# Optimization experiments

Measured on AMD Instinct MI355X. Metric: run time of the kernel, lower is better.

## Reference

```python
import jax, jax.numpy as jnp
import numpy as np

B, N, C = 32, 4096, 1152
TOPK_FRAC = 0.1


def setup_inputs() -> dict:
    key = jax.random.key(0)
    k1, k2 = jax.random.split(key)
    feature = jax.random.normal(k1, (B, N, C), dtype=jnp.float32)
    W = jax.random.normal(k2, (C,), dtype=jnp.float32) * 0.02  # conv1x1 weight [out=1, in=C, k=1] squeezed
    b = jnp.zeros((1,), dtype=jnp.float32)
    return {"feature": feature, "W": W, "b": b}


def reference(feature, W, b):
    # conv1x1 over [B, C, N] == per-patch dot product with W: [B, N]
    scores = jnp.einsum("bnc,c->bn", feature, W) + b[0]
    n = scores.shape[1]
    k = max(int(n * TOPK_FRAC), 1)  # static: 409
    topk_vals, _ = jax.lax.top_k(jnp.abs(scores), k)  # [B, k]
    per_sample = jnp.mean(topk_vals, axis=1)  # [B]
    # image_pyramid has a single level -> cat + mean over dim=1 is identity
    return [per_sample.reshape(-1, 1)]
```

## Files before the change

### kernel.cpp

```cpp
#include <hip/hip_runtime.h>

#define B_ 32
#define N_ 4096
#define C_ 1152
#define K_ 409

#define NBLK 2048
#define PATCH_PER_BLK ((B_ * N_) / NBLK)
#define ITERS (PATCH_PER_BLK / 4)

typedef float f32x4 __attribute__((ext_vector_type(4)));

__global__ __launch_bounds__(256) void score_abs_kernel(
    const float* __restrict__ feat, const float* __restrict__ W,
    const float* __restrict__ bias, float* __restrict__ absS) {
  __shared__ f32x4 Ws[C_ / 4];
  for (int i = threadIdx.x; i < C_ / 4; i += 256)
    Ws[i] = reinterpret_cast<const f32x4*>(W)[i];
  __syncthreads();

  const int wave = threadIdx.x >> 6;
  const int lane = threadIdx.x & 63;
  const float b0 = bias[0];

  const f32x4 w0 = Ws[lane];
  const f32x4 w1 = Ws[lane + 64];
  const f32x4 w2 = Ws[lane + 128];
  const f32x4 w3 = Ws[lane + 192];
  const f32x4 w4 = (lane < 32) ? Ws[lane + 256] : (f32x4)0.f;

  const int patch_base = blockIdx.x * PATCH_PER_BLK + wave;
#pragma unroll 4
  for (int it = 0; it < ITERS; ++it) {
    const int patch = patch_base + it * 4;
    const f32x4* f4 = reinterpret_cast<const f32x4*>(feat) + (size_t)patch * (C_ / 4);
    f32x4 vacc = __builtin_nontemporal_load(&f4[lane]) * w0;
    vacc += __builtin_nontemporal_load(&f4[lane + 64]) * w1;
    vacc += __builtin_nontemporal_load(&f4[lane + 128]) * w2;
    vacc += __builtin_nontemporal_load(&f4[lane + 192]) * w3;
    if (lane < 32) vacc += __builtin_nontemporal_load(&f4[lane + 256]) * w4;
    float acc = vacc[0] + vacc[1] + vacc[2] + vacc[3];
#pragma unroll
    for (int off = 32; off > 0; off >>= 1)
      acc += __shfl_down(acc, off, 64);
    if (lane == 0) absS[patch] = fabsf(acc + b0);
  }
}

__global__ __launch_bounds__(256) void topk_mean_kernel(
    const float* __restrict__ absS, float* __restrict__ out) {
  __shared__ float vals[N_];
  __shared__ unsigned hist[256];
  __shared__ unsigned cum[256];
  __shared__ unsigned s_sel[2];
  __shared__ unsigned s_cred[4];
  __shared__ float s_sredf[4];

  const int t = threadIdx.x;
  const int wv = t >> 6;
  const int ln = t & 63;
  const int b = blockIdx.x;
  const float4* row4 = reinterpret_cast<const float4*>(absS + (size_t)b * N_);
  for (int i = t; i < N_ / 4; i += 256)
    reinterpret_cast<float4*>(vals)[i] = row4[i];
  __syncthreads();

  unsigned prefix = 0;
  unsigned k = K_;
#pragma unroll
  for (int p = 0; p < 4; ++p) {
    const int shift = 24 - 8 * p;
    const unsigned hmask = (p == 0) ? 0u : (0xFFFFFFFFu << (shift + 8));
    hist[t] = 0;
    __syncthreads();
    for (int i = t; i < N_; i += 256) {
      const unsigned e = __float_as_uint(vals[i]);
      if ((e & hmask) == (prefix & hmask))
        atomicAdd(&hist[(e >> shift) & 255u], 1u);
    }
    __syncthreads();
    cum[t] = hist[t];
    __syncthreads();
#pragma unroll
    for (int off = 1; off < 256; off <<= 1) {
      const unsigned v = (t + off < 256) ? cum[t + off] : 0u;
      __syncthreads();
      cum[t] += v;
      __syncthreads();
    }
    const unsigned cnt_ge = cum[t];
    const unsigned cnt_gt = (t == 255) ? 0u : cum[t + 1];
    if (cnt_ge >= k && cnt_gt < k) {
      s_sel[0] = (unsigned)t;
      s_sel[1] = k - cnt_gt;
    }
    __syncthreads();
    prefix |= s_sel[0] << shift;
    k = s_sel[1];
    __syncthreads();
  }
  const float thr = __uint_as_float(prefix);

  float sum = 0.f;
  unsigned cgt = 0;
  for (int i = t; i < N_; i += 256) {
    const float v = vals[i];
    if (v > thr) { sum += v; cgt++; }
  }
#pragma unroll
  for (int off = 32; off > 0; off >>= 1) {
    sum += __shfl_down(sum, off, 64);
    cgt += __shfl_down(cgt, off, 64);
  }
  if (ln == 0) { s_cred[wv] = cgt; s_sredf[wv] = sum; }
  __syncthreads();
  if (t == 0) {
    const unsigned cg = s_cred[0] + s_cred[1] + s_cred[2] + s_cred[3];
    const float sg = s_sredf[0] + s_sredf[1] + s_sredf[2] + s_sredf[3];
    out[b] = (sg + (float)(K_ - (int)cg) * thr) / (float)K_;
  }
}

extern "C" void kernel_launch(void* const* d_in, const int* in_sizes, int n_in,
                              void* d_out, int out_size, void* d_ws, size_t ws_size,
                              hipStream_t stream) {
  const float* feat = (const float*)d_in[0];
  const float* W = (const float*)d_in[1];
  const float* bias = (const float*)d_in[2];
  float* out = (float*)d_out;
  float* absS = (float*)d_ws;

  score_abs_kernel<<<NBLK, 256, 0, stream>>>(feat, W, bias, absS);
  topk_mean_kernel<<<B_, 256, 0, stream>>>(absS, out);
}
```

Before: 108.2 us.

## Fuse scoring and top-k via last-block-per-row completion counter

New measurement: 322.3 us. 198% more time.

```diff
diff --git a/kernel.cpp b/kernel.cpp
--- a/kernel.cpp
+++ b/kernel.cpp
@@ -6,97 +6,116 @@
 #define K_ 409
 
 #define NBLK 2048
-#define PATCH_PER_BLK ((B_ * N_) / NBLK)
-#define ITERS (PATCH_PER_BLK / 4)
+#define PATCH_PER_BLK 64
+#define ITERS 16
+#define BLOCKS_PER_ROW 64
 
 typedef float f32x4 __attribute__((ext_vector_type(4)));
 
-__global__ __launch_bounds__(256) void score_abs_kernel(
+__global__ __launch_bounds__(256) void fused_kernel(
     const float* __restrict__ feat, const float* __restrict__ W,
-    const float* __restrict__ bias, float* __restrict__ absS) {
-  __shared__ f32x4 Ws[C_ / 4];
-  for (int i = threadIdx.x; i < C_ / 4; i += 256)
-    Ws[i] = reinterpret_cast<const f32x4*>(W)[i];
+    const float* __restrict__ bias, float* __restrict__ absS,
+    unsigned* __restrict__ cnt, float* __restrict__ out) {
+  __shared__ union {
+    f32x4 Ws[C_ / 4];
+    struct {
+      float vals[N_];
+      unsigned hist[256];
+      unsigned wsum[4];
+      unsigned sel[2];
+      float sredf[4];
+      unsigned cred[4];
+      int islast;
+    } tk;
+  } sh;
+
+  const int t = threadIdx.x;
+  const int wave = t >> 6;
+  const int lane = t & 63;
+
+  for (int i = t; i < C_ / 4; i += 256)
+    sh.Ws[i] = reinterpret_cast<const f32x4*>(W)[i];
   __syncthreads();
 
-  const int wave = threadIdx.x >> 6;
-  const int lane = threadIdx.x & 63;
   const float b0 = bias[0];
+  const f32x4 w0 = sh.Ws[lane];
+  const f32x4 w1 = sh.Ws[lane + 64];
+  const f32x4 w2 = sh.Ws[lane + 128];
+  const f32x4 w3 = sh.Ws[lane + 192];
+  const f32x4 w4 = (lane < 32) ? sh.Ws[256 + lane] : (f32x4)0.f;
 
-  const f32x4 w0 = Ws[lane];
-  const f32x4 w1 = Ws[lane + 64];
-  const f32x4 w2 = Ws[lane + 128];
-  const f32x4 w3 = Ws[lane + 192];
-  const f32x4 w4 = (lane < 32) ? Ws[lane + 256] : (f32x4)0.f;
-
-  const int patch_base = blockIdx.x * PATCH_PER_BLK + wave;
-#pragma unroll 4
+  const int patch0 = blockIdx.x * PATCH_PER_BLK + wave;
+  const f32x4* fbase = reinterpret_cast<const f32x4*>(feat);
+  float pacc[ITERS];
+#pragma unroll
   for (int it = 0; it < ITERS; ++it) {
-    const int patch = patch_base + it * 4;
-    const f32x4* f4 = reinterpret_cast<const f32x4*>(feat) + (size_t)patch * (C_ / 4);
+    const f32x4* f4 = fbase + (size_t)(patch0 + it * 4) * (C_ / 4);
     f32x4 vacc = __builtin_nontemporal_load(&f4[lane]) * w0;
     vacc += __builtin_nontemporal_load(&f4[lane + 64]) * w1;
     vacc += __builtin_nontemporal_load(&f4[lane + 128]) * w2;
     vacc += __builtin_nontemporal_load(&f4[lane + 192]) * w3;
-    if (lane < 32) vacc += __builtin_nontemporal_load(&f4[lane + 256]) * w4;
-    float acc = vacc[0] + vacc[1] + vacc[2] + vacc[3];
+    if (lane < 32) vacc += __builtin_nontemporal_load(&f4[256 + lane]) * w4;
+    pacc[it] = vacc[0] + vacc[1] + vacc[2] + vacc[3];
+  }
 #pragma unroll
-    for (int off = 32; off > 0; off >>= 1)
-      acc += __shfl_down(acc, off, 64);
-    if (lane == 0) absS[patch] = fabsf(acc + b0);
+  for (int it = 0; it < ITERS; ++it) {
+    float a = pacc[it];
+#pragma unroll
+    for (int off = 32; off > 0; off >>= 1) a += __shfl_down(a, off, 64);
+    if (lane == 0)
+      __hip_atomic_store(&absS[patch0 + it * 4], fabsf(a + b0),
+                         __ATOMIC_RELAXED, __HIP_MEMORY_SCOPE_AGENT);
   }
-}
 
-__global__ __launch_bounds__(256) void topk_mean_kernel(
-    const float* __restrict__ absS, float* __restrict__ out) {
-  __shared__ float vals[N_];
-  __shared__ unsigned hist[256];
-  __shared__ unsigned cum[256];
-  __shared__ unsigned s_sel[2];
-  __shared__ unsigned s_cred[4];
-  __shared__ float s_sredf[4];
+  const int row = blockIdx.x / BLOCKS_PER_ROW;
+  __threadfence();
+  __syncthreads();
+  if (t == 0) {
+    unsigned old = atomicAdd(&cnt[row], 1u);
+    sh.tk.islast = (old == BLOCKS_PER_ROW - 1);
+  }
+  __syncthreads();
+  if (!sh.tk.islast) return;
+  __threadfence();
 
-  const int t = threadIdx.x;
-  const int wv = t >> 6;
-  const int ln = t & 63;
-  const int b = blockIdx.x;
-  const float4* row4 = reinterpret_cast<const float4*>(absS + (size_t)b * N_);
-  for (int i = t; i < N_ / 4; i += 256)
-    reinterpret_cast<float4*>(vals)[i] = row4[i];
+  const float* rowp = absS + (size_t)row * N_;
+  for (int i = t; i < N_; i += 256)
+    sh.tk.vals[i] = __hip_atomic_load(&rowp[i], __ATOMIC_RELAXED,
+                                      __HIP_MEMORY_SCOPE_AGENT);
   __syncthreads();
 
-  unsigned prefix = 0;
-  unsigned k = K_;
+  unsigned prefix = 0, k = K_;
 #pragma unroll
   for (int p = 0; p < 4; ++p) {
     const int shift = 24 - 8 * p;
     const unsigned hmask = (p == 0) ? 0u : (0xFFFFFFFFu << (shift + 8));
-    hist[t] = 0;
+    sh.tk.hist[t] = 0;
     __syncthreads();
     for (int i = t; i < N_; i += 256) {
-      const unsigned e = __float_as_uint(vals[i]);
+      const unsigned e = __float_as_uint(sh.tk.vals[i]);
       if ((e & hmask) == (prefix & hmask))
-        atomicAdd(&hist[(e >> shift) & 255u], 1u);
+        atomicAdd(&sh.tk.hist[(e >> shift) & 255u], 1u);
     }
     __syncthreads();
-    cum[t] = hist[t];
+    const unsigned own = sh.tk.hist[t];
+    unsigned x = own;
+#pragma unroll
+    for (int off = 1; off < 64; off <<= 1) {
+      const unsigned v = __shfl_down(x, off, 64);
+      if (lane + off < 64) x += v;
+    }
+    if (lane == 0) sh.tk.wsum[wave] = x;
     __syncthreads();
-#pragma unroll
-    for (int off = 1; off < 256; off <<= 1) {
-      const unsigned v = (t + off < 256) ? cum[t + off] : 0u;
-      __syncthreads();
-      cum[t] += v;
-      __syncthreads();
-    }
-    const unsigned cnt_ge = cum[t];
-    const unsigned cnt_gt = (t == 255) ? 0u : cum[t + 1];
-    if (cnt_ge >= k && cnt_gt < k) {
-      s_sel[0] = (unsigned)t;
-      s_sel[1] = k - cnt_gt;
+    unsigned cum_ge = x;
+    for (int w = wave + 1; w < 4; ++w) cum_ge += sh.tk.wsum[w];
+    const unsigned cnt_gt = cum_ge - own;
+    if (cum_ge >= k && cnt_gt < k) {
+      sh.tk.sel[0] = (unsigned)t;
+      sh.tk.sel[1] = k - cnt_gt;
     }
     __syncthreads();
-    prefix |= s_sel[0] << shift;
-    k = s_sel[1];
+    prefix |= sh.tk.sel[0] << shift;
+    k = sh.tk.sel[1];
     __syncthreads();
   }
   const float thr = __uint_as_float(prefix);
@@ -104,7 +123,7 @@
   float sum = 0.f;
   unsigned cgt = 0;
   for (int i = t; i < N_; i += 256) {
-    const float v = vals[i];
+    const float v = sh.tk.vals[i];
     if (v > thr) { sum += v; cgt++; }
   }
 #pragma unroll
@@ -112,12 +131,12 @@
     sum += __shfl_down(sum, off, 64);
     cgt += __shfl_down(cgt, off, 64);
   }
-  if (ln == 0) { s_cred[wv] = cgt; s_sredf[wv] = sum; }
+  if (lane == 0) { sh.tk.cred[wave] = cgt; sh.tk.sredf[wave] = sum; }
   __syncthreads();
   if (t == 0) {
-    const unsigned cg = s_cred[0] + s_cred[1] + s_cred[2] + s_cred[3];
-    const float sg = s_sredf[0] + s_sredf[1] + s_sredf[2] + s_sredf[3];
-    out[b] = (sg + (float)(K_ - (int)cg) * thr) / (float)K_;
+    const unsigned cg = sh.tk.cred[0] + sh.tk.cred[1] + sh.tk.cred[2] + sh.tk.cred[3];
+    const float sg = sh.tk.sredf[0] + sh.tk.sredf[1] + sh.tk.sredf[2] + sh.tk.sredf[3];
+    out[row] = (sg + (float)(K_ - (int)cg) * thr) / (float)K_;
   }
 }
 
@@ -129,7 +148,8 @@
   const float* bias = (const float*)d_in[2];
   float* out = (float*)d_out;
   float* absS = (float*)d_ws;
+  unsigned* cnt = (unsigned*)((char*)d_ws + (size_t)B_ * N_ * sizeof(float));
 
-  score_abs_kernel<<<NBLK, 256, 0, stream>>>(feat, W, bias, absS);
-  topk_mean_kernel<<<B_, 256, 0, stream>>>(absS, out);
+  hipMemsetAsync(cnt, 0, B_ * sizeof(unsigned), stream);
+  fused_kernel<<<NBLK, 256, 0, stream>>>(feat, W, bias, absS, cnt, out);
 }
```
